# Kernel tuning notes

Hardware: AMD Instinct MI355X
Metric: run time of the kernel (lower is better)

## Reference

```python
import jax, jax.numpy as jnp
import numpy as np

B, N, M, C, H = 4, 2048, 2048, 1024, 16
D = C // H  # head_dim = 64
SCALE = D ** -0.5


def setup_inputs() -> dict:
    key = jax.random.key(0)
    ks = jax.random.split(key, 8)
    std = C ** -0.5
    return {
        "query": jax.random.normal(ks[0], (B, N, C), jnp.float32),
        "key": jax.random.normal(ks[1], (B, M, C), jnp.float32),
        "value": jax.random.normal(ks[2], (B, M, C), jnp.float32),
        "Wq": jax.random.normal(ks[3], (C, C), jnp.float32) * std,
        "Wk": jax.random.normal(ks[4], (C, C), jnp.float32) * std,
        "Wv": jax.random.normal(ks[5], (C, C), jnp.float32) * std,
        "Wp": jax.random.normal(ks[6], (C, C), jnp.float32) * std,
        "bp": jax.random.normal(ks[7], (C,), jnp.float32) * 0.01,
    }


def reference(query, key, value, Wq, Wk, Wv, Wp, bp):
    # Linear: y = x @ W.T (torch nn.Linear convention), no bias for q/k/v.
    # reshape (B,S,C)->(B,S,H,D)->(B,H,S,D)
    q = jnp.einsum('bnc,dc->bnd', query, Wq).reshape(B, N, H, D).transpose(0, 2, 1, 3)
    k = jnp.einsum('bmc,dc->bmd', key, Wk).reshape(B, M, H, D).transpose(0, 2, 1, 3)
    v = jnp.einsum('bmc,dc->bmd', value, Wv).reshape(B, M, H, D).transpose(0, 2, 1, 3)
    # scaled scores, softmax over keys
    attn = jnp.einsum('bhnd,bhmd->bhnm', q * SCALE, k)
    attn = jax.nn.softmax(attn, axis=-1)
    # attention output -> (B,N,C)
    x = jnp.einsum('bhnm,bhmd->bhnd', attn, v).transpose(0, 2, 1, 3).reshape(B, N, C)
    # output projection with bias
    return jnp.einsum('bnc,dc->bnd', x, Wp) + bp
```

## Files before the change

kernel.cpp:

```cpp
#include <hip/hip_runtime.h>
#include <stdint.h>

#define B_ 4
#define N_ 2048
#define M_ 2048
#define C_ 1024
#define H_ 16
#define D_ 64
#define SC_ (B_*N_*C_)
#define CC_ (C_*C_)

typedef unsigned short u16;
typedef __attribute__((ext_vector_type(8))) short short8;
typedef __attribute__((ext_vector_type(4))) short short4v;
typedef __attribute__((ext_vector_type(4))) float f32x4;

#if __has_builtin(__builtin_amdgcn_exp2f)
#define EXP2F __builtin_amdgcn_exp2f
#else
#define EXP2F exp2f
#endif

__device__ inline u16 f2bf(float f) {
    union { float f; uint32_t u; } v; v.f = f;
    uint32_t r = v.u + 0x7fffu + ((v.u >> 16) & 1u);
    return (u16)(r >> 16);
}

__device__ inline f32x4 mfma16x16x16_bf16(short4v a, short4v b, f32x4 c) {
#if __has_builtin(__builtin_amdgcn_mfma_f32_16x16x16bf16_1k)
    return __builtin_amdgcn_mfma_f32_16x16x16bf16_1k(a, b, c, 0, 0, 0);
#else
    asm volatile("v_mfma_f32_16x16x16_bf16 %0, %1, %2, %0"
                 : "+v"(c) : "v"(a), "v"(b));
    return c;
#endif
}

#define WAIT_BARRIER(N)                                         \
    do {                                                        \
        asm volatile("s_waitcnt vmcnt(" #N ")" ::: "memory");   \
        __builtin_amdgcn_s_barrier();                           \
        __builtin_amdgcn_sched_barrier(0);                      \
    } while (0)

__global__ __launch_bounds__(256) void convert_kernel(
    const float* __restrict__ q, const float* __restrict__ k, const float* __restrict__ v,
    const float* __restrict__ wq, const float* __restrict__ wk,
    const float* __restrict__ wv, const float* __restrict__ wp,
    u16* __restrict__ qf, u16* __restrict__ kf, u16* __restrict__ vf,
    u16* __restrict__ wqb, u16* __restrict__ wkb, u16* __restrict__ wvb, u16* __restrict__ wpb)
{
    const int SC4 = SC_ / 4;
    const int CC4 = CC_ / 4;
    const int total = 3 * SC4 + 4 * CC4;
    for (int i = blockIdx.x * 256 + threadIdx.x; i < total; i += gridDim.x * 256) {
        const float* src; u16* dst; int off;
        if (i < 3 * SC4) {
            int seg = i >> 21;
            off = (i & (SC4 - 1)) << 2;
            src = seg == 0 ? q : seg == 1 ? k : v;
            dst = seg == 0 ? qf : seg == 1 ? kf : vf;
        } else {
            int j = i - 3 * SC4;
            int seg = j >> 18;
            off = (j & (CC4 - 1)) << 2;
            src = seg == 0 ? wq : seg == 1 ? wk : seg == 2 ? wv : wp;
            dst = seg == 0 ? wqb : seg == 1 ? wkb : seg == 2 ? wvb : wpb;
        }
        float4 val = *(const float4*)(src + off);
        ushort4 h;
        h.x = f2bf(val.x); h.y = f2bf(val.y); h.z = f2bf(val.z); h.w = f2bf(val.w);
        *(ushort4*)(dst + off) = h;
    }
}

template<int OMODE>
__global__ __launch_bounds__(256) void gemm_lds(
    const u16* __restrict__ A, const u16* __restrict__ Wb,
    const float* __restrict__ bias, void* __restrict__ Op, float scale)
{
    const int K = 1024;
    __shared__ u16 SH[3 * 8192];
    const int tid = threadIdx.x;
    const int wid = tid >> 6, lane = tid & 63;
    const int quad = lane >> 4, l15 = lane & 15;
    const int f = blockIdx.x;
    const int m0 = (f & 63) * 128, n0 = (f >> 6) * 128;
    const int wm = (wid >> 1) * 64, wn = (wid & 1) * 64;

    size_t aoff[2], boff[2];
    int dsto[2];
#pragma unroll
    for (int i = 0; i < 2; ++i) {
        int s = tid + i * 256;
        int row = s >> 2, c8 = (s & 3) << 3;
        aoff[i] = (size_t)(m0 + row) * K + c8;
        boff[i] = (size_t)(n0 + row) * K + c8;
        dsto[i] = s * 8;
    }

    f32x4 acc[4][4];
#pragma unroll
    for (int i = 0; i < 4; ++i)
#pragma unroll
        for (int j = 0; j < 4; ++j) acc[i][j] = f32x4{0.f, 0.f, 0.f, 0.f};

#pragma unroll
    for (int t = 0; t < 2; ++t) {
        const int bo = t * 8192, k0 = t * 32;
#pragma unroll
        for (int i = 0; i < 2; ++i) {
            __builtin_amdgcn_global_load_lds(
                (const __attribute__((address_space(1))) void*)(A + aoff[i] + k0),
                (__attribute__((address_space(3))) void*)(SH + bo + dsto[i]), 16, 0, 0);
            __builtin_amdgcn_global_load_lds(
                (const __attribute__((address_space(1))) void*)(Wb + boff[i] + k0),
                (__attribute__((address_space(3))) void*)(SH + bo + 4096 + dsto[i]), 16, 0, 0);
        }
    }

    for (int it = 0; it < 32; ++it) {
        const int cur = (it % 3) * 8192;
        if (it < 31) WAIT_BARRIER(4);
        else         WAIT_BARRIER(0);
        if (it + 2 < 32) {
            const int nxt = ((it + 2) % 3) * 8192;
            const int k0n = (it + 2) * 32;
#pragma unroll
            for (int i = 0; i < 2; ++i) {
                __builtin_amdgcn_global_load_lds(
                    (const __attribute__((address_space(1))) void*)(A + aoff[i] + k0n),
                    (__attribute__((address_space(3))) void*)(SH + nxt + dsto[i]), 16, 0, 0);
                __builtin_amdgcn_global_load_lds(
                    (const __attribute__((address_space(1))) void*)(Wb + boff[i] + k0n),
                    (__attribute__((address_space(3))) void*)(SH + nxt + 4096 + dsto[i]), 16, 0, 0);
            }
        }
        short8 av[4], bv[4];
#pragma unroll
        for (int i = 0; i < 4; ++i)
            av[i] = *(const short8*)(SH + cur + (wm + i * 16 + l15) * 32 + quad * 8);
#pragma unroll
        for (int j = 0; j < 4; ++j)
            bv[j] = *(const short8*)(SH + cur + 4096 + (wn + j * 16 + l15) * 32 + quad * 8);
#pragma unroll
        for (int i = 0; i < 4; ++i)
#pragma unroll
            for (int j = 0; j < 4; ++j)
                acc[i][j] = __builtin_amdgcn_mfma_f32_16x16x32_bf16(av[i], bv[j], acc[i][j], 0, 0, 0);
    }

    if (OMODE == 2) {
#pragma unroll
        for (int j = 0; j < 4; ++j) {
            int col = n0 + wn + j * 16 + l15;
            float bb = bias[col];
#pragma unroll
            for (int i = 0; i < 4; ++i) {
                int row = m0 + wm + i * 16 + quad * 4;
#pragma unroll
                for (int r = 0; r < 4; ++r)
                    ((float*)Op)[(size_t)(row + r) * 1024 + col] = acc[i][j][r] * scale + bb;
            }
        }
    } else if (OMODE == 0) {
#pragma unroll
        for (int j = 0; j < 4; ++j) {
            int col = n0 + wn + j * 16 + l15;
#pragma unroll
            for (int i = 0; i < 4; ++i) {
                int row = m0 + wm + i * 16 + quad * 4;
#pragma unroll
                for (int r = 0; r < 4; ++r)
                    ((u16*)Op)[(size_t)(row + r) * 1024 + col] = f2bf(acc[i][j][r] * scale);
            }
        }
    } else {
#pragma unroll
        for (int j = 0; j < 4; ++j) {
            int col = n0 + wn + j * 16 + l15;
            int hh = col >> 6, dd = col & 63;
#pragma unroll
            for (int i = 0; i < 4; ++i) {
                int row = m0 + wm + i * 16 + quad * 4;
                int bb = row >> 11, mm = row & 2047;
                ushort4 hv;
                hv.x = f2bf(acc[i][j][0] * scale);
                hv.y = f2bf(acc[i][j][1] * scale);
                hv.z = f2bf(acc[i][j][2] * scale);
                hv.w = f2bf(acc[i][j][3] * scale);
                *(ushort4*)((u16*)Op + (((size_t)bb * 16 + hh) * 64 + dd) * 2048 + mm) = hv;
            }
        }
    }
}

__global__ __launch_bounds__(256, 3) void attn_kernel(
    const u16* __restrict__ qg, const u16* __restrict__ kg,
    const u16* __restrict__ vT, u16* __restrict__ xb)
{
    __shared__ __align__(16) u16 KV[2 * 8192];

    const int tid = threadIdx.x;
    const int wid = tid >> 6, lane = tid & 63;
    const int quad = lane >> 4, l15 = lane & 15;
    const int f = blockIdx.x;
    const int bh = f & 63, qt = f >> 6;
    const int b = bh >> 4, h = bh & 15;

    const u16* qbase = qg + ((size_t)(b * N_ + qt * 128 + wid * 32)) * C_ + h * 64;
    short8 qf[2][2];
#pragma unroll
    for (int qb2 = 0; qb2 < 2; ++qb2)
#pragma unroll
        for (int ch = 0; ch < 2; ++ch)
            qf[qb2][ch] = *(const short8*)(qbase + (size_t)(qb2 * 16 + l15) * C_ + ch * 32 + quad * 8);

    const u16* kptr[2];
    const u16* vptr[2];
    int dsto[2];
#pragma unroll
    for (int i = 0; i < 2; ++i) {
        int s = tid + i * 256;
        int row = s >> 3, g = s & 7;
        int gsw = g ^ (row & 7);
        kptr[i] = kg + ((size_t)(b * M_ + row)) * C_ + h * 64 + gsw * 8;
        vptr[i] = vT + (((size_t)b * 16 + h) * 64 + row) * M_ + gsw * 8;
        dsto[i] = s * 8;
    }

    f32x4 acc[4][2];
#pragma unroll
    for (int i = 0; i < 4; ++i)
#pragma unroll
        for (int j = 0; j < 2; ++j) acc[i][j] = f32x4{0.f, 0.f, 0.f, 0.f};
    float lsum[2] = {0.f, 0.f};

    const int swr = l15 & 7;
    const int kxo0 = ((0 * 4 + quad) ^ swr) << 3;
    const int kxo1 = ((1 * 4 + quad) ^ swr) << 3;
    int vbase[4];
#pragma unroll
    for (int db = 0; db < 4; ++db)
        vbase[db] = 4096 + (db * 16 + l15) * 64 + ((quad & 1) << 2);
    int vx[4];
#pragma unroll
    for (int kt = 0; kt < 4; ++kt)
        vx[kt] = ((kt * 2 + (quad >> 1)) ^ swr) << 3;

    union { short4v s; uint32_t u[2]; } pfrag[2], vfu;

#pragma unroll
    for (int i = 0; i < 2; ++i) {
        __builtin_amdgcn_global_load_lds(
            (const __attribute__((address_space(1))) void*)(kptr[i]),
            (__attribute__((address_space(3))) void*)(KV + dsto[i]), 16, 0, 0);
        __builtin_amdgcn_global_load_lds(
            (const __attribute__((address_space(1))) void*)(vptr[i]),
            (__attribute__((address_space(3))) void*)(KV + 4096 + dsto[i]), 16, 0, 0);
    }

    for (int it = 0; it < 32; ++it) {
        const int cur = (it & 1) * 8192;
        __syncthreads();
        if (it + 1 < 32) {
            const int nxt = ((it + 1) & 1) * 8192;
            const int kvn = (it + 1) * 64;
#pragma unroll
            for (int i = 0; i < 2; ++i) {
                __builtin_amdgcn_global_load_lds(
                    (const __attribute__((address_space(1))) void*)(kptr[i] + (size_t)kvn * C_),
                    (__attribute__((address_space(3))) void*)(KV + nxt + dsto[i]), 16, 0, 0);
                __builtin_amdgcn_global_load_lds(
                    (const __attribute__((address_space(1))) void*)(vptr[i] + kvn),
                    (__attribute__((address_space(3))) void*)(KV + nxt + 4096 + dsto[i]), 16, 0, 0);
            }
        }

#pragma unroll
        for (int kt = 0; kt < 4; ++kt) {
            const int kbase = cur + (kt * 16 + l15) * 64;
            short8 kf0 = *(const short8*)(KV + kbase + kxo0);
            short8 kf1 = *(const short8*)(KV + kbase + kxo1);
            f32x4 sc0 = f32x4{0.f, 0.f, 0.f, 0.f};
            f32x4 sc1 = f32x4{0.f, 0.f, 0.f, 0.f};
            sc0 = __builtin_amdgcn_mfma_f32_16x16x32_bf16(kf0, qf[0][0], sc0, 0, 0, 0);
            sc1 = __builtin_amdgcn_mfma_f32_16x16x32_bf16(kf0, qf[1][0], sc1, 0, 0, 0);
            sc0 = __builtin_amdgcn_mfma_f32_16x16x32_bf16(kf1, qf[0][1], sc0, 0, 0, 0);
            sc1 = __builtin_amdgcn_mfma_f32_16x16x32_bf16(kf1, qf[1][1], sc1, 0, 0, 0);

#pragma unroll
            for (int qb2 = 0; qb2 < 2; ++qb2) {
                const f32x4 sv = qb2 ? sc1 : sc0;
                float e0 = EXP2F(sv[0]);
                float e1 = EXP2F(sv[1]);
                float e2 = EXP2F(sv[2]);
                float e3 = EXP2F(sv[3]);
                lsum[qb2] += (e0 + e1) + (e2 + e3);
                pfrag[qb2].u[0] = __builtin_amdgcn_perm(__builtin_bit_cast(uint32_t, e1),
                                                        __builtin_bit_cast(uint32_t, e0), 0x07060302u);
                pfrag[qb2].u[1] = __builtin_amdgcn_perm(__builtin_bit_cast(uint32_t, e3),
                                                        __builtin_bit_cast(uint32_t, e2), 0x07060302u);
            }

#pragma unroll
            for (int db = 0; db < 4; ++db) {
                uint2 vlo = *(const uint2*)(KV + cur + vbase[db] + vx[kt]);
                vfu.u[0] = vlo.x; vfu.u[1] = vlo.y;
                acc[db][0] = mfma16x16x16_bf16(vfu.s, pfrag[0].s, acc[db][0]);
                acc[db][1] = mfma16x16x16_bf16(vfu.s, pfrag[1].s, acc[db][1]);
            }
        }
    }

    lsum[0] += __shfl_xor(lsum[0], 16);
    lsum[0] += __shfl_xor(lsum[0], 32);
    lsum[1] += __shfl_xor(lsum[1], 16);
    lsum[1] += __shfl_xor(lsum[1], 32);
    const float dinv[2] = {1.f / lsum[0], 1.f / lsum[1]};

#pragma unroll
    for (int qb2 = 0; qb2 < 2; ++qb2) {
        size_t ob = ((size_t)(b * N_ + qt * 128 + wid * 32 + qb2 * 16 + l15)) * C_ + h * 64;
#pragma unroll
        for (int db = 0; db < 4; ++db) {
            ushort4 st;
            st.x = f2bf(acc[db][qb2][0] * dinv[qb2]);
            st.y = f2bf(acc[db][qb2][1] * dinv[qb2]);
            st.z = f2bf(acc[db][qb2][2] * dinv[qb2]);
            st.w = f2bf(acc[db][qb2][3] * dinv[qb2]);
            *(ushort4*)(xb + ob + db * 16 + quad * 4) = st;
        }
    }
}

extern "C" void kernel_launch(void* const* d_in, const int* in_sizes, int n_in,
                              void* d_out, int out_size, void* d_ws, size_t ws_size,
                              hipStream_t stream) {
    const float* query = (const float*)d_in[0];
    const float* key   = (const float*)d_in[1];
    const float* value = (const float*)d_in[2];
    const float* Wq    = (const float*)d_in[3];
    const float* Wk    = (const float*)d_in[4];
    const float* Wv    = (const float*)d_in[5];
    const float* Wpm   = (const float*)d_in[6];
    const float* bp    = (const float*)d_in[7];
    float* out = (float*)d_out;

    u16* base = (u16*)d_ws;
    u16* qf  = base;
    u16* kf  = base + (size_t)SC_;
    u16* vf  = base + (size_t)2 * SC_;
    u16* kb  = base + (size_t)3 * SC_;
    u16* Wqb = base + (size_t)4 * SC_;
    u16* Wkb = Wqb + CC_;
    u16* Wvb = Wkb + CC_;
    u16* Wpb = Wvb + CC_;
    u16* vTp = kf;
    u16* qb  = vf;
    u16* xb  = qf;

    hipLaunchKernelGGL(convert_kernel, dim3(4096), dim3(256), 0, stream,
                       query, key, value, Wq, Wk, Wv, Wpm,
                       qf, kf, vf, Wqb, Wkb, Wvb, Wpb);

    dim3 gg(512), bb(256);
    hipLaunchKernelGGL((gemm_lds<0>), gg, bb, 0, stream, kf, Wkb, nullptr, (void*)kb, 1.0f);
    hipLaunchKernelGGL((gemm_lds<1>), gg, bb, 0, stream, vf, Wvb, nullptr, (void*)vTp, 1.0f);
    hipLaunchKernelGGL((gemm_lds<0>), gg, bb, 0, stream, qf, Wqb, nullptr, (void*)qb,
                       0.125f * 1.44269504088896340736f);

    hipLaunchKernelGGL(attn_kernel, dim3(1024), bb, 0, stream, qb, kb, vTp, xb);

    hipLaunchKernelGGL((gemm_lds<2>), gg, bb, 0, stream, xb, Wpb, bp, (void*)out, 1.0f);
}
```

Measured before the change: 344.5 us.

## Merge Q, K and V projection GEMMs into one grid launch

Replaces the three separate projection GEMM launches with a single 1536-block kernel that picks its input, weight, output and scale from the block index. The three projections can then fill the GPU together instead of running as three shorter waves, and launch gaps between them go away. Because the GEMMs now run concurrently, the transposed V output no longer aliases the K input buffer and is written to a fresh workspace region after the output-projection weights. It also adds a 3-blocks-per-CU launch bound. The new placement relies on the workspace being large enough past Wpb.

Result: faster. 330.7 us (-4.0%).

```diff
diff --git a/kernel.cpp b/kernel.cpp
--- a/kernel.cpp
+++ b/kernel.cpp
@@ -75,10 +75,124 @@
     }
 }
 
-template<int OMODE>
-__global__ __launch_bounds__(256) void gemm_lds(
+__global__ __launch_bounds__(256, 3) void gemm_qkv(
+    const u16* __restrict__ A0, const u16* __restrict__ W0, u16* __restrict__ O0,
+    const u16* __restrict__ A1, const u16* __restrict__ W1, u16* __restrict__ O1,
+    const u16* __restrict__ A2, const u16* __restrict__ W2, u16* __restrict__ O2,
+    float qscale)
+{
+    const int K = 1024;
+    __shared__ u16 SH[3 * 8192];
+    const int tid = threadIdx.x;
+    const int wid = tid >> 6, lane = tid & 63;
+    const int quad = lane >> 4, l15 = lane & 15;
+    const int gseg = blockIdx.x >> 9;
+    const int f = blockIdx.x & 511;
+    const u16* A  = gseg == 0 ? A0 : gseg == 1 ? A1 : A2;
+    const u16* Wb = gseg == 0 ? W0 : gseg == 1 ? W1 : W2;
+    u16* Op       = gseg == 0 ? O0 : gseg == 1 ? O1 : O2;
+    const float scale = gseg == 2 ? qscale : 1.0f;
+
+    const int m0 = (f & 63) * 128, n0 = (f >> 6) * 128;
+    const int wm = (wid >> 1) * 64, wn = (wid & 1) * 64;
+
+    size_t aoff[2], boff[2];
+    int dsto[2];
+#pragma unroll
+    for (int i = 0; i < 2; ++i) {
+        int s = tid + i * 256;
+        int row = s >> 2, c8 = (s & 3) << 3;
+        aoff[i] = (size_t)(m0 + row) * K + c8;
+        boff[i] = (size_t)(n0 + row) * K + c8;
+        dsto[i] = s * 8;
+    }
+
+    f32x4 acc[4][4];
+#pragma unroll
+    for (int i = 0; i < 4; ++i)
+#pragma unroll
+        for (int j = 0; j < 4; ++j) acc[i][j] = f32x4{0.f, 0.f, 0.f, 0.f};
+
+#pragma unroll
+    for (int t = 0; t < 2; ++t) {
+        const int bo = t * 8192, k0 = t * 32;
+#pragma unroll
+        for (int i = 0; i < 2; ++i) {
+            __builtin_amdgcn_global_load_lds(
+                (const __attribute__((address_space(1))) void*)(A + aoff[i] + k0),
+                (__attribute__((address_space(3))) void*)(SH + bo + dsto[i]), 16, 0, 0);
+            __builtin_amdgcn_global_load_lds(
+                (const __attribute__((address_space(1))) void*)(Wb + boff[i] + k0),
+                (__attribute__((address_space(3))) void*)(SH + bo + 4096 + dsto[i]), 16, 0, 0);
+        }
+    }
+
+    for (int it = 0; it < 32; ++it) {
+        const int cur = (it % 3) * 8192;
+        if (it < 31) WAIT_BARRIER(4);
+        else         WAIT_BARRIER(0);
+        if (it + 2 < 32) {
+            const int nxt = ((it + 2) % 3) * 8192;
+            const int k0n = (it + 2) * 32;
+#pragma unroll
+            for (int i = 0; i < 2; ++i) {
+                __builtin_amdgcn_global_load_lds(
+                    (const __attribute__((address_space(1))) void*)(A + aoff[i] + k0n),
+                    (__attribute__((address_space(3))) void*)(SH + nxt + dsto[i]), 16, 0, 0);
+                __builtin_amdgcn_global_load_lds(
+                    (const __attribute__((address_space(1))) void*)(Wb + boff[i] + k0n),
+                    (__attribute__((address_space(3))) void*)(SH + nxt + 4096 + dsto[i]), 16, 0, 0);
+            }
+        }
+        short8 av[4], bv[4];
+#pragma unroll
+        for (int i = 0; i < 4; ++i)
+            av[i] = *(const short8*)(SH + cur + (wm + i * 16 + l15) * 32 + quad * 8);
+#pragma unroll
+        for (int j = 0; j < 4; ++j)
+            bv[j] = *(const short8*)(SH + cur + 4096 + (wn + j * 16 + l15) * 32 + quad * 8);
+#pragma unroll
+        for (int i = 0; i < 4; ++i)
+#pragma unroll
+            for (int j = 0; j < 4; ++j)
+                acc[i][j] = __builtin_amdgcn_mfma_f32_16x16x32_bf16(av[i], bv[j], acc[i][j], 0, 0, 0);
+    }
+
+    if (gseg == 1) {
+#pragma unroll
+        for (int j = 0; j < 4; ++j) {
+            int col = n0 + wn + j * 16 + l15;
+            int hh = col >> 6, dd = col & 63;
+#pragma unroll
+            for (int i = 0; i < 4; ++i) {
+                int row = m0 + wm + i * 16 + quad * 4;
+                int bb = row >> 11, mm = row & 2047;
+                ushort4 hv;
+                hv.x = f2bf(acc[i][j][0]);
+                hv.y = f2bf(acc[i][j][1]);
+                hv.z = f2bf(acc[i][j][2]);
+                hv.w = f2bf(acc[i][j][3]);
+                *(ushort4*)(Op + (((size_t)bb * 16 + hh) * 64 + dd) * 2048 + mm) = hv;
+            }
+        }
+    } else {
+#pragma unroll
+        for (int j = 0; j < 4; ++j) {
+            int col = n0 + wn + j * 16 + l15;
+#pragma unroll
+            for (int i = 0; i < 4; ++i) {
+                int row = m0 + wm + i * 16 + quad * 4;
+#pragma unroll
+                for (int r = 0; r < 4; ++r)
+                    Op[(size_t)(row + r) * 1024 + col] = f2bf(acc[i][j][r] * scale);
+            }
+        }
+    }
+}
+
+__global__ __launch_bounds__(256) void gemm_p(
     const u16* __restrict__ A, const u16* __restrict__ Wb,
-    const float* __restrict__ bias, void* __restrict__ Op, float scale)
+    const float* __restrict__ bias, float* __restrict__ Op)
 {
     const int K = 1024;
     __shared__ u16 SH[3 * 8192];
@@ -151,47 +265,16 @@
                 acc[i][j] = __builtin_amdgcn_mfma_f32_16x16x32_bf16(av[i], bv[j], acc[i][j], 0, 0, 0);
     }
 
-    if (OMODE == 2) {
-#pragma unroll
-        for (int j = 0; j < 4; ++j) {
-            int col = n0 + wn + j * 16 + l15;
-            float bb = bias[col];
-#pragma unroll
-            for (int i = 0; i < 4; ++i) {
-                int row = m0 + wm + i * 16 + quad * 4;
-#pragma unroll
-                for (int r = 0; r < 4; ++r)
-                    ((float*)Op)[(size_t)(row + r) * 1024 + col] = acc[i][j][r] * scale + bb;
-            }
-        }
-    } else if (OMODE == 0) {
-#pragma unroll
-        for (int j = 0; j < 4; ++j) {
-            int col = n0 + wn + j * 16 + l15;
-#pragma unroll
-            for (int i = 0; i < 4; ++i) {
-                int row = m0 + wm + i * 16 + quad * 4;
-#pragma unroll
-                for (int r = 0; r < 4; ++r)
-                    ((u16*)Op)[(size_t)(row + r) * 1024 + col] = f2bf(acc[i][j][r] * scale);
-            }
-        }
-    } else {
-#pragma unroll
-        for (int j = 0; j < 4; ++j) {
-            int col = n0 + wn + j * 16 + l15;
-            int hh = col >> 6, dd = col & 63;
-#pragma unroll
-            for (int i = 0; i < 4; ++i) {
-                int row = m0 + wm + i * 16 + quad * 4;
-                int bb = row >> 11, mm = row & 2047;
-                ushort4 hv;
-                hv.x = f2bf(acc[i][j][0] * scale);
-                hv.y = f2bf(acc[i][j][1] * scale);
-                hv.z = f2bf(acc[i][j][2] * scale);
-                hv.w = f2bf(acc[i][j][3] * scale);
-                *(ushort4*)((u16*)Op + (((size_t)bb * 16 + hh) * 64 + dd) * 2048 + mm) = hv;
-            }
+#pragma unroll
+    for (int j = 0; j < 4; ++j) {
+        int col = n0 + wn + j * 16 + l15;
+        float bb = bias[col];
+#pragma unroll
+        for (int i = 0; i < 4; ++i) {
+            int row = m0 + wm + i * 16 + quad * 4;
+#pragma unroll
+            for (int r = 0; r < 4; ++r)
+                Op[(size_t)(row + r) * 1024 + col] = acc[i][j][r] + bb;
         }
     }
 }
@@ -365,13 +448,15 @@
                        query, key, value, Wq, Wk, Wv, Wpm,
                        qf, kf, vf, Wqb, Wkb, Wvb, Wpb);
 
-    dim3 gg(512), bb(256);
-    hipLaunchKernelGGL((gemm_lds<0>), gg, bb, 0, stream, kf, Wkb, nullptr, (void*)kb, 1.0f);
-    hipLaunchKernelGGL((gemm_lds<1>), gg, bb, 0, stream, vf, Wvb, nullptr, (void*)vTp, 1.0f);
-    hipLaunchKernelGGL((gemm_lds<0>), gg, bb, 0, stream, qf, Wqb, nullptr, (void*)qb,
+    hipLaunchKernelGGL(gemm_qkv, dim3(1536), dim3(256), 0, stream,
+                       kf, Wkb, kb,
+                       vf, Wvb, Wpb + CC_,
+                       qf, Wqb, qb,
                        0.125f * 1.44269504088896340736f);
 
-    hipLaunchKernelGGL(attn_kernel, dim3(1024), bb, 0, stream, qb, kb, vTp, xb);
-
-    hipLaunchKernelGGL((gemm_lds<2>), gg, bb, 0, stream, xb, Wpb, bp, (void*)out, 1.0f);
-}
+    u16* vTr = Wpb + CC_;
+
+    hipLaunchKernelGGL(attn_kernel, dim3(1024), dim3(256), 0, stream, qb, kb, vTr, xb);
+
+    hipLaunchKernelGGL(gemm_p, dim3(512), dim3(256), 0, stream, xb, Wpb, bp, out);
+}
```
